# Kernel optimization log

Measured on AMD Instinct MI355X. Metric: run time of the kernel, lower is better.

## Reference

```python
import jax, jax.numpy as jnp
import numpy as np

L, H, N = 4096, 256, 64  # seq_len, hidden_size, hippo_n
EPS = 1e-5


def setup_inputs() -> dict:
    key = jax.random.key(0)
    ks = jax.random.split(key, 8)
    x = jax.random.normal(ks[0], (L, H), jnp.float32)
    # S4D-Lin style initialization for the diagonal SSM (H independent SSMs of state size N)
    Lambda_re = -0.5 * jnp.ones((H, N), jnp.float32)
    Lambda_im = jnp.tile(jnp.pi * jnp.arange(N, dtype=jnp.float32), (H, 1))
    B_re = jnp.ones((H, N), jnp.float32)
    B_im = jnp.zeros((H, N), jnp.float32)
    C_re = jax.random.normal(ks[1], (H, N), jnp.float32) * (0.5 ** 0.5)
    C_im = jax.random.normal(ks[2], (H, N), jnp.float32) * (0.5 ** 0.5)
    D = jax.random.normal(ks[3], (H,), jnp.float32)
    log_step = jax.random.uniform(ks[4], (H,), jnp.float32,
                                  minval=jnp.log(0.001), maxval=jnp.log(0.1))
    ln_w = jnp.ones((H,), jnp.float32)
    ln_b = jnp.zeros((H,), jnp.float32)
    sc = 1.0 / jnp.sqrt(jnp.float32(H))
    W1 = jax.random.normal(ks[5], (H, H), jnp.float32) * sc
    b1 = jnp.zeros((H,), jnp.float32)
    W2 = jax.random.normal(ks[6], (H, H), jnp.float32) * sc
    b2 = jnp.zeros((H,), jnp.float32)
    return {"x": x, "Lambda_re": Lambda_re, "Lambda_im": Lambda_im,
            "B_re": B_re, "B_im": B_im, "C_re": C_re, "C_im": C_im,
            "D": D, "log_step": log_step, "ln_w": ln_w, "ln_b": ln_b,
            "W1": W1, "b1": b1, "W2": W2, "b2": b2}


def reference(x, Lambda_re, Lambda_im, B_re, B_im, C_re, C_im, D, log_step,
              ln_w, ln_b, W1, b1, W2, b2):
    skip = x
    # per-token LayerNorm over the H feature axis (eqx.nn.LayerNorm, eps=1e-5)
    mu = jnp.mean(x, axis=-1, keepdims=True)
    var = jnp.mean(jnp.square(x - mu), axis=-1, keepdims=True)
    xn = (x - mu) / jnp.sqrt(var + EPS) * ln_w + ln_b  # [L, H]

    # ZOH discretization of the diagonal SSM (the cell.ssm(L) step)
    Lam = Lambda_re + 1j * Lambda_im                     # [H, N] complex64
    dt = jnp.exp(log_step)[:, None]                      # [H, 1]
    Ab = jnp.exp(Lam * dt)                               # [H, N]
    Bb = (Ab - 1.0) / Lam * (B_re + 1j * B_im)           # [H, N]
    C = C_re + 1j * C_im                                 # [H, N]

    def step(s, u):  # s: [H, N] complex state, u: [H] input at one time step
        s = Ab * s + Bb * u[:, None]
        y = 2.0 * jnp.einsum('hn,hn->h', C, s).real + D * u
        return s, y

    s0 = jnp.zeros((H, N), jnp.complex64)
    hidden, ys = jax.lax.scan(step, s0, xn)              # ys: [L, H]

    g = jax.nn.gelu(ys)
    out = (g @ W1.T + b1) * jax.nn.sigmoid(g @ W2.T + b2)  # GLU epilogue
    return (hidden, skip + out)
```

## Files before the change

kernel.cpp:

```cpp
#include <hip/hip_runtime.h>
#include <hip/hip_bf16.h>

#define LSEQ 4096
#define HDIM 256
#define NS   64
#define PC   32
#define MC   128

typedef __attribute__((ext_vector_type(8))) short short8;
typedef __attribute__((ext_vector_type(4))) float floatx4;

__device__ __forceinline__ short b16(float x) {
    __hip_bfloat16 h = __float2bfloat16(x);
    return *(reinterpret_cast<short*>(&h));
}
__device__ __forceinline__ unsigned int pk2(float a, float b) {
    return (unsigned int)(unsigned short)b16(a) | ((unsigned int)(unsigned short)b16(b) << 16);
}
__device__ __forceinline__ void cmul(float& xr, float& xi, float yr, float yi) {
    float r = xr * yr - xi * yi;
    float i = xr * yi + xi * yr;
    xr = r; xi = i;
}

__global__ __launch_bounds__(256) void k_pre(const float* __restrict__ x,
                                             const float* __restrict__ lnw,
                                             const float* __restrict__ lnb,
                                             const float* __restrict__ W1,
                                             const float* __restrict__ W2,
                                             float* __restrict__ xnT,
                                             unsigned short* __restrict__ w1b,
                                             unsigned short* __restrict__ w2b) {
    int t = threadIdx.x;
    if (blockIdx.x >= 256) {
        int g = (blockIdx.x - 256) * 256 + t;
        float4 a = ((const float4*)W1)[g];
        float4 c = ((const float4*)W2)[g];
        ushort4 o1, o2;
        o1.x = (unsigned short)b16(a.x); o1.y = (unsigned short)b16(a.y);
        o1.z = (unsigned short)b16(a.z); o1.w = (unsigned short)b16(a.w);
        o2.x = (unsigned short)b16(c.x); o2.y = (unsigned short)b16(c.y);
        o2.z = (unsigned short)b16(c.z); o2.w = (unsigned short)b16(c.w);
        ((ushort4*)w1b)[g] = o1;
        ((ushort4*)w2b)[g] = o2;
        return;
    }
    __shared__ float tile[16][257];
    __shared__ float smu[16], srs[16];
    int l0 = blockIdx.x * 16;
#pragma unroll
    for (int i = 0; i < 16; ++i)
        tile[i][t] = x[(size_t)(l0 + i) * HDIM + t];
    __syncthreads();
    int wv = t >> 6, lane = t & 63;
#pragma unroll
    for (int k = 0; k < 4; ++k) {
        int i = wv * 4 + k;
        float s = 0.f, s2 = 0.f;
#pragma unroll
        for (int q = 0; q < 4; ++q) {
            float v = tile[i][lane + 64 * q];
            s += v; s2 += v * v;
        }
#pragma unroll
        for (int o = 32; o; o >>= 1) {
            s  += __shfl_xor(s, o);
            s2 += __shfl_xor(s2, o);
        }
        if (lane == 0) {
            float m = s * (1.0f / HDIM);
            smu[i] = m;
            srs[i] = rsqrtf(s2 * (1.0f / HDIM) - m * m + 1e-5f);
        }
    }
    __syncthreads();
    float wh = lnw[t], bh = lnb[t];
    float o[16];
#pragma unroll
    for (int i = 0; i < 16; ++i)
        o[i] = (tile[i][t] - smu[i]) * srs[i] * wh + bh;
    float4* dst = (float4*)(xnT + (size_t)t * LSEQ + l0);
#pragma unroll
    for (int k = 0; k < 4; ++k)
        dst[k] = make_float4(o[4 * k], o[4 * k + 1], o[4 * k + 2], o[4 * k + 3]);
}

__device__ __forceinline__ void ssm_consts(const float* Lre, const float* Lim,
                                           const float* Bre, const float* Bim,
                                           float dt, int idx,
                                           float& are, float& aim, float& bre, float& bim) {
    float lre = Lre[idx], lim = Lim[idx];
    float er = expf(lre * dt);
    float sa, ca;
    sincosf(lim * dt, &sa, &ca);
    are = er * ca; aim = er * sa;
    float inv = 1.0f / (lre * lre + lim * lim);
    float nre = are - 1.0f, nim = aim;
    float tre = (nre * lre + nim * lim) * inv;
    float tim = (nim * lre - nre * lim) * inv;
    float br = Bre[idx], bi = Bim[idx];
    bre = tre * br - tim * bi;
    bim = tre * bi + tim * br;
}

__global__ __launch_bounds__(1024) void k_scan(const float* __restrict__ xnT,
                                               const float* __restrict__ Lre,
                                               const float* __restrict__ Lim,
                                               const float* __restrict__ Bre,
                                               const float* __restrict__ Bim,
                                               const float* __restrict__ Cre,
                                               const float* __restrict__ Cim,
                                               const float* __restrict__ Dv,
                                               const float* __restrict__ lstep,
                                               __hip_bfloat16* __restrict__ gb,
                                               float* __restrict__ hid,
                                               int interleaved) {
    __shared__ __align__(16) unsigned char ldsb[60672];
    short* ubf = (short*)(ldsb);
    short* Tm  = (short*)(ldsb + 8704);
    float* Ff  = (float*)(ldsb + 43520);
    short* S0s = (short*)(ldsb + 43520);
    float* Kt  = (float*)(ldsb + 60160);

    int h = blockIdx.x;
    int tid = threadIdx.x;
    int wv = __builtin_amdgcn_readfirstlane(tid) >> 6;
    int lane = tid & 63;
    int l15 = lane & 15, q = lane >> 4;
    int mt = wv >> 1, nt = wv & 1;
    const float* uh = xnT + (size_t)h * LSEQ;

    float dt = expf(lstep[h]);
    float Dh = Dv[h];

    float are, aim, bre, bim;
    ssm_consts(Lre, Lim, Bre, Bim, dt, h * NS + lane, are, aim, bre, bim);
    float cre = Cre[h * NS + lane], cim = Cim[h * NS + lane];

    float A2r = are, A2i = aim;   cmul(A2r, A2i, are, aim);
    float A4r = A2r, A4i = A2i;   cmul(A4r, A4i, A2r, A2i);
    float A8r = A4r, A8i = A4i;   cmul(A8r, A8i, A4r, A4i);
    float A16r = A8r, A16i = A8i;  cmul(A16r, A16i, A8r, A8i);
    float A32r = A16r, A32i = A16i; cmul(A32r, A32i, A16r, A16i);
    float A64r = A32r, A64i = A32i; cmul(A64r, A64i, A32r, A32i);

    {
        int i4 = tid * 4;
        float4 v = *(const float4*)(uh + i4);
        int c = i4 >> 7, col = i4 & 127;
        unsigned int* d = (unsigned int*)(ubf + c * 136 + col);
        d[0] = pk2(v.x, v.y);
        d[1] = pk2(v.z, v.w);
    }

    {
        float cbre = cre * bre - cim * bim;
        float cbim = cre * bim + cim * bre;
        float pr = 1.f, pi = 0.f;
        if (wv & 1) cmul(pr, pi, A8r, A8i);
        if (wv & 2) cmul(pr, pi, A16r, A16i);
        if (wv & 4) cmul(pr, pi, A32r, A32i);
        if (wv & 8) cmul(pr, pi, A64r, A64i);
#pragma unroll
        for (int i = 0; i < 8; ++i) {
            float kj = 2.f * (cbre * pr - cbim * pi);
#pragma unroll
            for (int o = 1; o <= 32; o <<= 1) kj += __shfl_xor(kj, o);
            if (lane == 0) Kt[8 * wv + i] = kj;
            cmul(pr, pi, are, aim);
        }
    }

    {
        int v = 15 - wv;
        float pr = 1.f, pi = 0.f;
        if (v & 1) cmul(pr, pi, A8r, A8i);
        if (v & 2) cmul(pr, pi, A16r, A16i);
        if (v & 4) cmul(pr, pi, A32r, A32i);
        if (v & 8) cmul(pr, pi, A64r, A64i);
        short8 rr, ri;
#pragma unroll
        for (int i = 0; i < 8; ++i) {
            rr[7 - i] = b16(bre * pr - bim * pi);
            ri[7 - i] = b16(bre * pi + bim * pr);
            cmul(pr, pi, are, aim);
        }
        *(short8*)(Tm + lane * 136 + 8 * wv) = rr;
        *(short8*)(Tm + (64 + lane) * 136 + 8 * wv) = ri;
    }
    __syncthreads();

    {
        floatx4 fa = (floatx4){0.f, 0.f, 0.f, 0.f};
#pragma unroll
        for (int ks = 0; ks < 4; ++ks) {
            short8 am = *(short8*)(Tm + (16 * mt + l15) * 136 + 32 * ks + 8 * q);
            short8 bu = *(short8*)(ubf + (16 * nt + l15) * 136 + 32 * ks + 8 * q);
            fa = __builtin_amdgcn_mfma_f32_16x16x32_bf16(am, bu, fa, 0, 0, 0);
        }
        int c = 16 * nt + l15;
        float* fp = Ff + c * 130;
        int sbase = 16 * mt + 4 * q;
#pragma unroll
        for (int reg = 0; reg < 4; ++reg) {
            int s = sbase + reg;
            fp[(mt < 4) ? s : (1 + s)] = fa[reg];
        }
    }
    __syncthreads();

    if (wv != 0) {
#pragma unroll
        for (int it = 0; it < 18; ++it) {
            int idx = it * 960 + (tid - 64);
            if (idx < 128 * 128) {
                int row = idx >> 7, col = idx & 127;
                float kv = Kt[(row - col) & 127];
                Tm[row * 136 + col] = (col <= row) ? b16(kv) : (short)0;
            }
        }
    } else {
        float a128r = A64r, a128i = A64i;
        cmul(a128r, a128i, A64r, A64i);
        float sre = 0.f, sim = 0.f;
        for (int c = 0; c < PC; ++c) {
            float fre = Ff[c * 130 + lane];
            float fim = Ff[c * 130 + 65 + lane];
            ((unsigned int*)(ldsb + 43520 + 272 * c))[lane] = pk2(sre, sim);
            float nr = fmaf(a128r, sre, fmaf(-a128i, sim, fre));
            float ni = fmaf(a128r, sim, fmaf( a128i, sre, fim));
            sre = nr; sim = ni;
        }
        if (interleaved) {
            ((float2*)hid)[h * NS + lane] = make_float2(sre, sim);
        } else {
            hid[h * NS + lane] = sre;
        }
    }
    __syncthreads();

    floatx4 Y = (floatx4){0.f, 0.f, 0.f, 0.f};
#pragma unroll
    for (int ks = 0; ks < 4; ++ks) {
        short8 ta = *(short8*)(Tm + (16 * mt + l15) * 136 + 32 * ks + 8 * q);
        short8 bu = *(short8*)(ubf + (16 * nt + l15) * 136 + 32 * ks + 8 * q);
        Y = __builtin_amdgcn_mfma_f32_16x16x32_bf16(ta, bu, Y, 0, 0, 0);
    }
    __syncthreads();

    {
        float pr = are, pi = aim;
        if (wv & 1) cmul(pr, pi, A8r, A8i);
        if (wv & 2) cmul(pr, pi, A16r, A16i);
        if (wv & 4) cmul(pr, pi, A32r, A32i);
        if (wv & 8) cmul(pr, pi, A64r, A64i);
#pragma unroll
        for (int i = 0; i < 8; ++i) {
            int t = 8 * wv + i;
            float er =  2.f * (cre * pr - cim * pi);
            float en = -2.f * (cre * pi + cim * pr);
            ((unsigned int*)(ldsb + 8704 + 272 * t))[lane] = pk2(er, en);
            cmul(pr, pi, are, aim);
        }
    }
    __syncthreads();

#pragma unroll
    for (int ks = 0; ks < 4; ++ks) {
        short8 ea = *(short8*)(Tm + (16 * mt + l15) * 136 + 32 * ks + 8 * q);
        short8 sf = *(short8*)(S0s + (16 * nt + l15) * 136 + 32 * ks + 8 * q);
        Y = __builtin_amdgcn_mfma_f32_16x16x32_bf16(ea, sf, Y, 0, 0, 0);
    }

    {
        int c = 16 * nt + l15;
#pragma unroll
        for (int reg = 0; reg < 4; ++reg) {
            int t = 16 * mt + 4 * q + reg;
            int l = c * MC + t;
            float u = uh[l];
            float y = Y[reg] + Dh * u;
            float z = 0.7978845608028654f * fmaf(0.044715f, y * y * y, y);
            float e = __expf(2.f * z);
            float th = 1.f - 2.f / (e + 1.f);
            float gg = 0.5f * y * (1.f + th);
            gb[((size_t)l << 8) + h] = __float2bfloat16(gg);
        }
    }
}

__global__ __launch_bounds__(64) void k_glu_mfma(const unsigned short* __restrict__ gbs,
                                                 const unsigned short* __restrict__ w1b,
                                                 const unsigned short* __restrict__ w2b,
                                                 const float* __restrict__ b1v,
                                                 const float* __restrict__ b2v,
                                                 const float* __restrict__ x,
                                                 float* __restrict__ out) {
    int bx = blockIdx.x;
    int m0 = (bx >> 4) * 32;
    int n0 = (bx & 15) * 16;
    int lane = threadIdx.x;
    int t = lane & 15, q = lane >> 4;

    floatx4 acc[2][2];
    acc[0][0] = (floatx4){0,0,0,0}; acc[0][1] = (floatx4){0,0,0,0};
    acc[1][0] = (floatx4){0,0,0,0}; acc[1][1] = (floatx4){0,0,0,0};

    const unsigned short* A0 = gbs + (size_t)(m0 + t) * HDIM + q * 8;
    const unsigned short* A1 = A0 + 16 * HDIM;
    const unsigned short* B1 = w1b + (size_t)(n0 + t) * HDIM + q * 8;
    const unsigned short* B2 = w2b + (size_t)(n0 + t) * HDIM + q * 8;

#pragma unroll
    for (int ks = 0; ks < 8; ++ks) {
        int off = ks * 32;
        short8 a0 = *(const short8*)(A0 + off);
        short8 a1 = *(const short8*)(A1 + off);
        short8 b1 = *(const short8*)(B1 + off);
        short8 b2 = *(const short8*)(B2 + off);
        acc[0][0] = __builtin_amdgcn_mfma_f32_16x16x32_bf16(a0, b1, acc[0][0], 0, 0, 0);
        acc[1][0] = __builtin_amdgcn_mfma_f32_16x16x32_bf16(a1, b1, acc[1][0], 0, 0, 0);
        acc[0][1] = __builtin_amdgcn_mfma_f32_16x16x32_bf16(a0, b2, acc[0][1], 0, 0, 0);
        acc[1][1] = __builtin_amdgcn_mfma_f32_16x16x32_bf16(a1, b2, acc[1][1], 0, 0, 0);
    }

    int hh = n0 + t;
    float bb1 = b1v[hh], bb2 = b2v[hh];
#pragma unroll
    for (int mt = 0; mt < 2; ++mt) {
#pragma unroll
        for (int reg = 0; reg < 4; ++reg) {
            int l = m0 + mt * 16 + q * 4 + reg;
            float a  = acc[mt][0][reg] + bb1;
            float sg = 1.f / (1.f + __expf(-(acc[mt][1][reg] + bb2)));
            out[(size_t)l * HDIM + hh] = fmaf(a, sg, x[(size_t)l * HDIM + hh]);
        }
    }
}

extern "C" void kernel_launch(void* const* d_in, const int* in_sizes, int n_in,
                              void* d_out, int out_size, void* d_ws, size_t ws_size,
                              hipStream_t stream) {
    (void)in_sizes; (void)n_in; (void)ws_size;
    const float* x     = (const float*)d_in[0];
    const float* Lre   = (const float*)d_in[1];
    const float* Lim   = (const float*)d_in[2];
    const float* Bre   = (const float*)d_in[3];
    const float* Bim   = (const float*)d_in[4];
    const float* Cre   = (const float*)d_in[5];
    const float* Cim   = (const float*)d_in[6];
    const float* Dv    = (const float*)d_in[7];
    const float* lstep = (const float*)d_in[8];
    const float* lnw   = (const float*)d_in[9];
    const float* lnb   = (const float*)d_in[10];
    const float* W1    = (const float*)d_in[11];
    const float* b1    = (const float*)d_in[12];
    const float* W2    = (const float*)d_in[13];
    const float* b2    = (const float*)d_in[14];

    float* ws   = (float*)d_ws;
    float* xnT  = ws;
    unsigned short* gb  = (unsigned short*)(xnT + (size_t)HDIM * LSEQ);
    unsigned short* w1b = gb + (size_t)LSEQ * HDIM;
    unsigned short* w2b = w1b + HDIM * HDIM;

    int interleaved = (out_size == LSEQ * HDIM + 2 * HDIM * NS) ? 1 : 0;
    float* hid  = (float*)d_out;
    float* outp = (float*)d_out + (interleaved ? 2 * HDIM * NS : HDIM * NS);

    k_pre      <<<256 + 64, 256, 0, stream>>>(x, lnw, lnb, W1, W2, xnT, w1b, w2b);
    k_scan     <<<HDIM, 1024, 0, stream>>>(xnT, Lre, Lim, Bre, Bim, Cre, Cim,
                                           Dv, lstep, (__hip_bfloat16*)gb, hid, interleaved);
    k_glu_mfma <<<128 * 16, 64, 0, stream>>>(gb, w1b, w2b, b1, b2, x, outp);
}
```

Before: 114.9 us.

## Build Toeplitz operand in registers and overlap state scan with emission writes

Drops the 128x128 lower-triangular Toeplitz matrix stored in LDS and builds each MFMA A-fragment directly in registers from the kernel vector Kt. With that LDS region free, waves 1-15 write the C*A^t emission rows while wave 0 runs the sequential chunk-state scan, which removes two block barriers. The cost is per-lane scattered LDS reads of Kt plus extra bf16 conversions inside the MFMA loop, and the emission powers are now built with a different multiplication chain.

```diff
diff --git a/kernel.cpp b/kernel.cpp
--- a/kernel.cpp
+++ b/kernel.cpp
@@ -117,7 +117,7 @@
                                                int interleaved) {
     __shared__ __align__(16) unsigned char ldsb[60672];
     short* ubf = (short*)(ldsb);
-    short* Tm  = (short*)(ldsb + 8704);
+    short* Xm  = (short*)(ldsb + 8704);
     float* Ff  = (float*)(ldsb + 43520);
     short* S0s = (short*)(ldsb + 43520);
     float* Kt  = (float*)(ldsb + 60160);
@@ -185,8 +185,8 @@
             ri[7 - i] = b16(bre * pi + bim * pr);
             cmul(pr, pi, are, aim);
         }
-        *(short8*)(Tm + lane * 136 + 8 * wv) = rr;
-        *(short8*)(Tm + (64 + lane) * 136 + 8 * wv) = ri;
+        *(short8*)(Xm + lane * 136 + 8 * wv) = rr;
+        *(short8*)(Xm + (64 + lane) * 136 + 8 * wv) = ri;
     }
     __syncthreads();
 
@@ -194,7 +194,7 @@
         floatx4 fa = (floatx4){0.f, 0.f, 0.f, 0.f};
 #pragma unroll
         for (int ks = 0; ks < 4; ++ks) {
-            short8 am = *(short8*)(Tm + (16 * mt + l15) * 136 + 32 * ks + 8 * q);
+            short8 am = *(short8*)(Xm + (16 * mt + l15) * 136 + 32 * ks + 8 * q);
             short8 bu = *(short8*)(ubf + (16 * nt + l15) * 136 + 32 * ks + 8 * q);
             fa = __builtin_amdgcn_mfma_f32_16x16x32_bf16(am, bu, fa, 0, 0, 0);
         }
@@ -209,17 +209,7 @@
     }
     __syncthreads();
 
-    if (wv != 0) {
-#pragma unroll
-        for (int it = 0; it < 18; ++it) {
-            int idx = it * 960 + (tid - 64);
-            if (idx < 128 * 128) {
-                int row = idx >> 7, col = idx & 127;
-                float kv = Kt[(row - col) & 127];
-                Tm[row * 136 + col] = (col <= row) ? b16(kv) : (short)0;
-            }
-        }
-    } else {
+    if (wv == 0) {
         float a128r = A64r, a128i = A64i;
         cmul(a128r, a128i, A64r, A64i);
         float sre = 0.f, sim = 0.f;
@@ -236,38 +226,49 @@
         } else {
             hid[h * NS + lane] = sre;
         }
-    }
-    __syncthreads();
+    } else {
+        float A15r = A8r, A15i = A8i;
+        cmul(A15r, A15i, A4r, A4i);
+        cmul(A15r, A15i, A2r, A2i);
+        cmul(A15r, A15i, are, aim);
+        float pr = 1.f, pi = 0.f;
+        if (wv & 1) cmul(pr, pi, are, aim);
+        if (wv & 2) cmul(pr, pi, A2r, A2i);
+        if (wv & 4) cmul(pr, pi, A4r, A4i);
+        if (wv & 8) cmul(pr, pi, A8r, A8i);
+#pragma unroll
+        for (int i = 0; i < 9; ++i) {
+            int t = (wv - 1) + 15 * i;
+            if (t < 128) {
+                float er =  2.f * (cre * pr - cim * pi);
+                float en = -2.f * (cre * pi + cim * pr);
+                ((unsigned int*)(ldsb + 8704 + 272 * t))[lane] = pk2(er, en);
+            }
+            cmul(pr, pi, A15r, A15i);
+        }
+    }
 
     floatx4 Y = (floatx4){0.f, 0.f, 0.f, 0.f};
+    {
+        int row = 16 * mt + l15;
+#pragma unroll
+        for (int ks = 0; ks < 4; ++ks) {
+            short8 ta;
+#pragma unroll
+            for (int e = 0; e < 8; ++e) {
+                int col = 32 * ks + 8 * q + e;
+                float kv = Kt[(row - col) & 127];
+                ta[e] = (col <= row) ? b16(kv) : (short)0;
+            }
+            short8 bu = *(short8*)(ubf + (16 * nt + l15) * 136 + 32 * ks + 8 * q);
+            Y = __builtin_amdgcn_mfma_f32_16x16x32_bf16(ta, bu, Y, 0, 0, 0);
+        }
+    }
+    __syncthreads();
+
 #pragma unroll
     for (int ks = 0; ks < 4; ++ks) {
-        short8 ta = *(short8*)(Tm + (16 * mt + l15) * 136 + 32 * ks + 8 * q);
-        short8 bu = *(short8*)(ubf + (16 * nt + l15) * 136 + 32 * ks + 8 * q);
-        Y = __builtin_amdgcn_mfma_f32_16x16x32_bf16(ta, bu, Y, 0, 0, 0);
-    }
-    __syncthreads();
-
-    {
-        float pr = are, pi = aim;
-        if (wv & 1) cmul(pr, pi, A8r, A8i);
-        if (wv & 2) cmul(pr, pi, A16r, A16i);
-        if (wv & 4) cmul(pr, pi, A32r, A32i);
-        if (wv & 8) cmul(pr, pi, A64r, A64i);
-#pragma unroll
-        for (int i = 0; i < 8; ++i) {
-            int t = 8 * wv + i;
-            float er =  2.f * (cre * pr - cim * pi);
-            float en = -2.f * (cre * pi + cim * pr);
-            ((unsigned int*)(ldsb + 8704 + 272 * t))[lane] = pk2(er, en);
-            cmul(pr, pi, are, aim);
-        }
-    }
-    __syncthreads();
-
-#pragma unroll
-    for (int ks = 0; ks < 4; ++ks) {
-        short8 ea = *(short8*)(Tm + (16 * mt + l15) * 136 + 32 * ks + 8 * q);
+        short8 ea = *(short8*)(Xm + (16 * mt + l15) * 136 + 32 * ks + 8 * q);
         short8 sf = *(short8*)(S0s + (16 * nt + l15) * 136 + 32 * ks + 8 * q);
         Y = __builtin_amdgcn_mfma_f32_16x16x32_bf16(ea, sf, Y, 0, 0, 0);
     }
```

Result: no change. 115.9 us (+0.8%).
